# Kernel tuning notes

Hardware: AMD Instinct MI355X
Metric: run time of the kernel (lower is better)

## Reference

```python
import jax, jax.numpy as jnp
import numpy as np

EPS = 1e-36
N, F, C = 1024, 128, 2
P_DIM, BOND, SPACING, M_DIM = 4, 32, 8, 16
EMB_DIM = P_DIM ** C  # 16
NORM_INTERVAL = 1
STD = 0.55
N_BIG = (F + SPACING - 1) // SPACING   # 16 sites with output leg m=M_DIM
N_SMALL = F - N_BIG                    # 112 sites with m=1


def trig_embedding(x, p):
    # x: [N, F, C] in [0,1] -> [N, F, p**C]
    half = p // 2
    ks = 2.0 ** jnp.arange(1, half + 1, dtype=x.dtype)   # [2, 4, ...]
    ang = jnp.pi * x[..., None] / ks                     # [N,F,C,half]
    emb = jnp.stack([jnp.sin(ang), jnp.cos(ang)], -1)    # [N,F,C,half,2] -> sin1,cos1,sin2,cos2,...
    emb = emb.reshape(x.shape + (p,)) / float(np.sqrt(half))
    cur = emb[..., 0, :]
    for c in range(1, x.shape[-1]):                      # tensor product over channels
        cur = (cur[..., :, None] * emb[..., c, None, :]).reshape(x.shape[0], x.shape[1], -1)
    return cur


def build_mpo(w_big, w_small, sites, spacing):
    # Reassemble per-site MPO tensors (Dl, e, m, Dr); boundary bonds sliced to 1.
    mpo = []
    for n in range(sites):
        A = w_big[n // spacing] if n % spacing == 0 else w_small[n - n // spacing - 1]
        if n == 0:
            A = A[:1]
        if n == sites - 1:
            A = A[..., :1]
        mpo.append(A)
    return mpo


def _rescale(cur, log_norm):
    s = jnp.max(jnp.abs(cur))
    return cur / s, log_norm + jnp.log(s + EPS)


def log_partition_mpo(mpo):
    # log of squared F-norm of the MPO via zig-zag self-contraction with rescaling.
    sites = len(mpo)
    cur = mpo[0][0]                                   # (e, m, r); left bond (=1) squeezed
    log_norm = jnp.zeros((), cur.dtype)
    for i in range(sites - 1):
        if NORM_INTERVAL is not None and i % NORM_INTERVAL == 0:
            cur, log_norm = _rescale(cur, log_norm)
        if i == 0:
            cur = jnp.einsum('emf,emg->fg', cur, mpo[0][0])      # contract phys legs of site 0 copies
        else:
            cur = jnp.einsum('demf,demg->fg', cur, mpo[i])       # absorb copy-chain site i
        cur = jnp.einsum('fg,femh->gemh', cur, mpo[i + 1])       # absorb original-chain site i+1
    cur = jnp.einsum('demf,demg->fg', cur, mpo[-1])              # (1,1)
    return jnp.log(cur.reshape(()) + EPS) + log_norm


def sample_logit(emb_row, mpo):
    # emb_row: [F, e]. psi_n = sum_e A_n[l,e,m,r] emb[n,e]; logit = log ||psi||^2 (zig-zag + rescale).
    sites = len(mpo)
    psi_prev = jnp.einsum('emr,e->mr', mpo[0][0], emb_row[0])
    cur = psi_prev
    log_norm = jnp.zeros((), cur.dtype)
    for i in range(sites - 1):
        if NORM_INTERVAL is not None and i % NORM_INTERVAL == 0:
            cur, log_norm = _rescale(cur, log_norm)
        if i == 0:
            cur = jnp.einsum('mf,mg->fg', cur, psi_prev)
        else:
            cur = jnp.einsum('dmf,dmg->fg', cur, psi_prev)
        psi_prev = jnp.einsum('lemr,e->lmr', mpo[i + 1], emb_row[i + 1])
        cur = jnp.einsum('fg,fmh->gmh', cur, psi_prev)
    cur = jnp.einsum('dmf,dmg->fg', cur, psi_prev)               # (1,1)
    return jnp.log(cur.reshape(()) + EPS) + log_norm


def forward(x, w_big, w_small):
    emb = trig_embedding(x, P_DIM)                    # [N, F, EMB_DIM]
    mpo = build_mpo(w_big, w_small, F, SPACING)
    log_Z = log_partition_mpo(mpo)
    logits = jax.vmap(lambda e: sample_logit(e, mpo))(emb)   # [N]
    return logits, log_Z


def setup_inputs() -> dict:
    key = jax.random.key(0)
    k1, k2, k3 = jax.random.split(key, 3)
    x = jax.random.uniform(k1, (N, F, C), dtype=jnp.float32)
    w_big = STD * jax.random.normal(k2, (N_BIG, BOND, EMB_DIM, M_DIM, BOND), dtype=jnp.float32)
    w_small = STD * jax.random.normal(k3, (N_SMALL, BOND, EMB_DIM, 1, BOND), dtype=jnp.float32)
    return {"x": x, "w_big": w_big, "w_small": w_small}


def reference(x, w_big, w_small):
    return forward(x, w_big, w_small)
```

## Files before the change

kernel.cpp:

```cpp
#include <hip/hip_runtime.h>

typedef __attribute__((ext_vector_type(8)))  short  s16x8;
typedef __attribute__((ext_vector_type(8)))  __bf16 bf16x8;
typedef __attribute__((ext_vector_type(16))) float  f32x16;
typedef __attribute__((ext_vector_type(4)))  unsigned int u32x4;

#define EPSF 1e-36f

static __device__ __forceinline__ f32x16 MFMA(s16x8 a, s16x8 b, f32x16 c) {
  return __builtin_amdgcn_mfma_f32_32x32x16_bf16(
      __builtin_bit_cast(bf16x8, a), __builtin_bit_cast(bf16x8, b), c, 0, 0, 0);
}

static __device__ __forceinline__ short f2bf(float f) {
  unsigned u = __builtin_bit_cast(unsigned, f);
  u = (u + 0x7FFFu + ((u >> 16) & 1u)) >> 16;
  return (short)u;
}

static __device__ __forceinline__ unsigned pkf(float a, float b) {
  return (unsigned)(unsigned short)f2bf(a) | ((unsigned)(unsigned short)f2bf(b) << 16);
}

static __device__ __forceinline__ void redistR(const f32x16 d, float sc, int h,
                                               s16x8& f0, s16x8& f1) {
  unsigned pk[8];
#pragma unroll
  for (int q = 0; q < 8; ++q) pk[q] = pkf(d[2 * q] * sc, d[2 * q + 1] * sc);
  unsigned s0 = h ? pk[0] : pk[2];
  unsigned s1 = h ? pk[1] : pk[3];
  unsigned s2 = h ? pk[4] : pk[6];
  unsigned s3 = h ? pk[5] : pk[7];
  unsigned r0 = (unsigned)__shfl_xor((int)s0, 32);
  unsigned r1 = (unsigned)__shfl_xor((int)s1, 32);
  unsigned r2 = (unsigned)__shfl_xor((int)s2, 32);
  unsigned r3 = (unsigned)__shfl_xor((int)s3, 32);
  u32x4 a, b;
  a.x = h ? r0 : pk[0]; a.y = h ? r1 : pk[1]; a.z = h ? pk[2] : r0; a.w = h ? pk[3] : r1;
  b.x = h ? r2 : pk[4]; b.y = h ? r3 : pk[5]; b.z = h ? pk[6] : r2; b.w = h ? pk[7] : r3;
  f0 = __builtin_bit_cast(s16x8, a);
  f1 = __builtin_bit_cast(s16x8, b);
}

static __device__ __forceinline__ void decodeStep(int sig, int& site, int& m, int& off) {
  int g = sig / 23, o = sig - g * 23;
  if (o < 16) { site = 8 * g; m = o; off = g * 376832 + o * 16384; }
  else { site = 8 * g + (o - 15); m = 0; off = g * 376832 + 262144 + (o - 16) * 16384; }
}

extern "C" __global__ void prep_emb_k(const float* __restrict__ x, float* __restrict__ Em) {
  int id = blockIdx.x * 256 + threadIdx.x;
  int site = id >> 10, n = id & 1023;
  float x0 = x[(n * 128 + site) * 2 + 0];
  float x1 = x[(n * 128 + site) * 2 + 1];
  const float P5 = 1.57079632679f, P25 = 0.785398163397f, R = 0.70710678118f;
  float u[4] = {sinf(P5 * x0) * R, cosf(P5 * x0) * R, sinf(P25 * x0) * R, cosf(P25 * x0) * R};
  float v[4] = {sinf(P5 * x1) * R, cosf(P5 * x1) * R, sinf(P25 * x1) * R, cosf(P25 * x1) * R};
#pragma unroll
  for (int a = 0; a < 4; ++a) {
    float4 o;
    o.x = u[a] * v[0]; o.y = u[a] * v[1]; o.z = u[a] * v[2]; o.w = u[a] * v[3];
    *(float4*)&Em[id * 16 + a * 4] = o;
  }
}

extern "C" __global__ void prep_w_k(const float* __restrict__ wb, const float* __restrict__ wsm,
                                    short* __restrict__ As, short* __restrict__ As2) {
  int site = blockIdx.x;
  bool big = (site & 7) == 0;
  int nE = big ? 262144 : 16384;
  int nb = (site + 7) >> 3;
  int bs = nb * 262144 + (site - nb) * 16384;
  int kb = site >> 3;
  int ksm = site - kb - 1;
  for (int i = threadIdx.x; i < nE; i += 256) {
    int e = i & 15, r = (i >> 4) & 31, l = (i >> 9) & 31, m = i >> 14;
    float val = big ? wb[(((kb * 32 + l) * 16 + e) * 16 + m) * 32 + r]
                    : wsm[((ksm * 32 + l) * 16 + e) * 32 + r];
    if (site == 0 && l != 0) val = 0.f;
    if (site == 127 && r != 0) val = 0.f;
    short bv = f2bf(val);
    As2[bs + i] = bv;
    As[bs + ((m * 32 + r) * 16 + e) * 32 + l] = bv;
  }
}

extern "C" __global__ void __launch_bounds__(256, 1)
tn_main(const short* __restrict__ As, const short* __restrict__ As2,
        const float* __restrict__ Em, float* __restrict__ out) {
  __shared__ __align__(16) char smem[40960];
  const int tid = threadIdx.x;
  const int lane = tid & 63;
  const int w = tid >> 6;
  const int c31 = lane & 31;
  const int h = lane >> 5;
  const f32x16 Z = {0.f,0.f,0.f,0.f,0.f,0.f,0.f,0.f,0.f,0.f,0.f,0.f,0.f,0.f,0.f,0.f};

  if (blockIdx.x < 256) {
    const int n0 = blockIdx.x * 4;
    s16x8 Mf0 = {0,0,0,0,0,0,0,0}, Mf1 = {0,0,0,0,0,0,0,0};
    if (lane == 0) Mf0[0] = (short)0x3F80;
    f32x16 Macc = Z;
    float log_norm = 0.f;
    s16x8 Ef = {0,0,0,0,0,0,0,0};

    auto stage = [&](int sig2) {
      int st2, m2, off2; decodeStep(sig2, st2, m2, off2);
      const char* src = (const char*)As2 + (size_t)off2 * 2;
#pragma unroll
      for (int k = 0; k < 8; ++k) {
        int GL = (k * 4 + w) * 64 + lane;
        int gs = (GL & ~63) | ((GL & 63) ^ ((GL >> 6) & 7));
        __builtin_amdgcn_global_load_lds((const unsigned int*)(src + gs * 16),
                                         (unsigned int*)(smem + (k * 4 + w) * 1024),
                                         16, 0, 0);
      }
    };

    stage(0);
    __syncthreads();

#pragma unroll 1
    for (int sig = 0; sig < 368; ++sig) {
      int site, m, off; decodeStep(sig, site, m, off); (void)off;

      if (m == 0) {
        float4 q0 = {0.f,0.f,0.f,0.f}, q1 = {0.f,0.f,0.f,0.f};
        if (c31 < 4) {
          const float* ep = Em + ((size_t)site * 1024 + n0 + c31) * 16 + 8 * h;
          q0 = *(const float4*)ep;
          q1 = *(const float4*)(ep + 4);
        }
        u32x4 ef;
        ef.x = pkf(q0.x, q0.y); ef.y = pkf(q0.z, q0.w);
        ef.z = pkf(q1.x, q1.y); ef.w = pkf(q1.z, q1.w);
        Ef = __builtin_bit_cast(s16x8, ef);
      }

      unsigned* barea = (unsigned*)(smem + 32768);
#pragma unroll
      for (int t = 0; t < 4; ++t) {
        const int lA = 8 * w + 2 * t;
        const int lB = lA + 1;
        s16x8 WA = *(const s16x8*)(smem + lA * 1024 + (((c31 * 2 + h) ^ (lA & 7)) << 4));
        s16x8 WB = *(const s16x8*)(smem + lB * 1024 + (((c31 * 2 + h) ^ (lB & 7)) << 4));
        f32x16 DA = MFMA(Ef, WA, Z);
        f32x16 DB = MFMA(Ef, WB, Z);
        if (h == 0) {
          const int pr = (4 * w + t) ^ (c31 & 15);
#pragma unroll
          for (int q = 0; q < 4; ++q)
            barea[q * 512 + c31 * 16 + pr] = pkf(DA[q], DB[q]);
        }
      }
      __syncthreads();

      if (sig + 1 < 368) stage(sig + 1);

      const unsigned* ba = (const unsigned*)(smem + 32768) + w * 512 + c31 * 16;
      u32x4 b0v, b1v;
#pragma unroll
      for (int i = 0; i < 4; ++i) ((unsigned*)&b0v)[i] = ba[(4 * h + i) ^ (c31 & 15)];
#pragma unroll
      for (int i = 0; i < 4; ++i) ((unsigned*)&b1v)[i] = ba[(8 + 4 * h + i) ^ (c31 & 15)];
      s16x8 c0 = __builtin_bit_cast(s16x8, b0v);
      s16x8 c1 = __builtin_bit_cast(s16x8, b1v);

      f32x16 D1 = MFMA(Mf0, c0, Z);
      D1 = MFMA(Mf1, c1, D1);
      s16x8 Cf0, Cf1;
      redistR(D1, 1.f, h, Cf0, Cf1);
      if (m == 0) Macc = Z;
      Macc = MFMA(c0, Cf0, Macc);
      Macc = MFMA(c1, Cf1, Macc);

      bool lastM = (m == (((site & 7) == 0) ? 15 : 0));
      if (lastM) {
        if (site < 127) {
          float s = fabsf(Macc[0]);
#pragma unroll
          for (int j = 1; j < 16; ++j) s = fmaxf(s, fabsf(Macc[j]));
#pragma unroll
          for (int off2 = 32; off2 >= 1; off2 >>= 1) s = fmaxf(s, __shfl_xor(s, off2));
          float inv = 1.f / (s + EPSF);
          log_norm += logf(s + EPSF);
          redistR(Macc, inv, h, Mf0, Mf1);
        } else {
          if (lane == 0) out[n0 + w] = logf(fmaxf(Macc[0], 0.f) + EPSF) + log_norm;
        }
      }
      __syncthreads();
    }
  } else {
    float* red = (float*)smem;
    s16x8 Mf0 = {0,0,0,0,0,0,0,0}, Mf1 = {0,0,0,0,0,0,0,0};
    if (lane == 0) Mf0[0] = (short)0x3F80;
    f32x16 Macc = Z;
    float log_norm = 0.f;
#pragma unroll 1
    for (int sig = 0; sig < 368; ++sig) {
      int site, m, off; decodeStep(sig, site, m, off);
      if (m == 0) Macc = Z;
      s16x8 pa[4], pb[4];
#pragma unroll
      for (int q = 0; q < 4; ++q) {
        int e = 4 * w + q;
        const short* ap = As + off + (c31 * 16 + e) * 32;
        pa[q] = *(const s16x8*)(ap + 8 * h);
        pb[q] = *(const s16x8*)(ap + 16 + 8 * h);
      }
#pragma unroll
      for (int q = 0; q < 4; ++q) {
        f32x16 D1 = MFMA(Mf0, pa[q], Z);
        D1 = MFMA(Mf1, pb[q], D1);
        s16x8 Cf0, Cf1;
        redistR(D1, 1.f, h, Cf0, Cf1);
        Macc = MFMA(pa[q], Cf0, Macc);
        Macc = MFMA(pb[q], Cf1, Macc);
      }
      bool lastM = (m == (((site & 7) == 0) ? 15 : 0));
      if (lastM) {
        float* myr = red + w * 1056;
#pragma unroll
        for (int reg = 0; reg < 16; ++reg) {
          int row = (reg & 3) + 8 * (reg >> 2) + 4 * h;
          myr[row * 33 + c31] = Macc[reg];
        }
        __syncthreads();
        f32x16 tot;
#pragma unroll
        for (int reg = 0; reg < 16; ++reg) {
          int row = (reg & 3) + 8 * (reg >> 2) + 4 * h;
          int idx = row * 33 + c31;
          tot[reg] = red[idx] + red[1056 + idx] + red[2112 + idx] + red[3168 + idx];
        }
        float s = fabsf(tot[0]);
#pragma unroll
        for (int j = 1; j < 16; ++j) s = fmaxf(s, fabsf(tot[j]));
#pragma unroll
        for (int off2 = 32; off2 >= 1; off2 >>= 1) s = fmaxf(s, __shfl_xor(s, off2));
        __syncthreads();
        if (site < 127) {
          float inv = 1.f / (s + EPSF);
          log_norm += logf(s + EPSF);
          redistR(tot, inv, h, Mf0, Mf1);
        } else {
          if (tid == 0) out[1024] = logf(fmaxf(tot[0], 0.f) + EPSF) + log_norm;
        }
      }
    }
  }
}

extern "C" void kernel_launch(void* const* d_in, const int* in_sizes, int n_in,
                              void* d_out, int out_size, void* d_ws, size_t ws_size,
                              hipStream_t stream) {
  (void)in_sizes; (void)n_in; (void)out_size; (void)ws_size;
  const float* x   = (const float*)d_in[0];
  const float* wb  = (const float*)d_in[1];
  const float* wsm = (const float*)d_in[2];
  char* ws = (char*)d_ws;
  short* As  = (short*)ws;
  short* As2 = (short*)(ws + 12058624);
  float* Em  = (float*)(ws + 24117248);
  float* out = (float*)d_out;

  prep_emb_k<<<512, 256, 0, stream>>>(x, Em);
  prep_w_k<<<128, 256, 0, stream>>>(wb, wsm, As, As2);
  tn_main<<<257, 256, 0, stream>>>(As, As2, Em, out);
}
```

Measured before the change: 1.265 ms.

## Warp-specialize sample blocks into producer/consumer waves with double-buffered LDS

Blocks grow to 512 threads. In the sample blocks, four producer waves load MPO tiles into registers and compute the embedding-contracted slices into a double-buffered LDS area, while four consumer waves run the serial bond-chain MFMA updates one step behind. All embeddings for the block are preloaded into LDS up front, and the partition-function block now spreads its work over 8 waves with ping-pong partial buffers, so it needs one barrier per step instead of two. The aim is to hide global load latency and the producer MFMA work behind the serial consumer chain, at the cost of more registers, more LDS and a barrier every step.

Result: slower. 1.365 ms (+7.8%).

```diff
diff --git a/kernel.cpp b/kernel.cpp
--- a/kernel.cpp
+++ b/kernel.cpp
@@ -85,10 +85,10 @@
   }
 }
 
-extern "C" __global__ void __launch_bounds__(256, 1)
+extern "C" __global__ void __launch_bounds__(512, 1)
 tn_main(const short* __restrict__ As, const short* __restrict__ As2,
         const float* __restrict__ Em, float* __restrict__ out) {
-  __shared__ __align__(16) char smem[40960];
+  __shared__ __align__(16) char smem[67584];
   const int tid = threadIdx.x;
   const int lane = tid & 63;
   const int w = tid >> 6;
@@ -97,150 +97,175 @@
   const f32x16 Z = {0.f,0.f,0.f,0.f,0.f,0.f,0.f,0.f,0.f,0.f,0.f,0.f,0.f,0.f,0.f,0.f};
 
   if (blockIdx.x < 256) {
+    unsigned* bufU = (unsigned*)smem;
+    float* EmL = (float*)(smem + 16384);
     const int n0 = blockIdx.x * 4;
+
+    {
+      float4* dst = (float4*)EmL;
+#pragma unroll
+      for (int k = 0; k < 4; ++k) {
+        int j = k * 512 + tid;
+        int st = j >> 4, s = (j >> 2) & 3, q = j & 3;
+        dst[j] = *((const float4*)(Em + ((size_t)st * 1024 + n0 + s) * 16) + q);
+      }
+    }
+    __syncthreads();
+
+    if (w < 4) {
+      s16x8 Mf0 = {0,0,0,0,0,0,0,0}, Mf1 = {0,0,0,0,0,0,0,0};
+      if (lane == 0) Mf0[0] = (short)0x3F80;
+      f32x16 Macc = Z;
+      float log_norm = 0.f;
+
+      __syncthreads();
+#pragma unroll 1
+      for (int sig = 0; sig < 368; ++sig) {
+        int site, m, off; decodeStep(sig, site, m, off); (void)off;
+        const unsigned* bu = bufU + (sig & 1) * 2048 + w * 512 + c31;
+        u32x4 b0v, b1v;
+#pragma unroll
+        for (int j = 0; j < 4; ++j) ((unsigned*)&b0v)[j] = bu[(4 * h + j) * 32];
+#pragma unroll
+        for (int j = 0; j < 4; ++j) ((unsigned*)&b1v)[j] = bu[(8 + 4 * h + j) * 32];
+        s16x8 c0 = __builtin_bit_cast(s16x8, b0v);
+        s16x8 c1 = __builtin_bit_cast(s16x8, b1v);
+
+        f32x16 D1 = MFMA(Mf0, c0, Z);
+        D1 = MFMA(Mf1, c1, D1);
+        s16x8 Cf0, Cf1;
+        redistR(D1, 1.f, h, Cf0, Cf1);
+        if (m == 0) Macc = Z;
+        Macc = MFMA(c0, Cf0, Macc);
+        Macc = MFMA(c1, Cf1, Macc);
+
+        bool lastM = (m == (((site & 7) == 0) ? 15 : 0));
+        if (lastM) {
+          if (site < 127) {
+            float s = fabsf(Macc[0]);
+#pragma unroll
+            for (int j = 1; j < 16; ++j) s = fmaxf(s, fabsf(Macc[j]));
+#pragma unroll
+            for (int off2 = 32; off2 >= 1; off2 >>= 1) s = fmaxf(s, __shfl_xor(s, off2));
+            float inv = 1.f / (s + EPSF);
+            log_norm += logf(s + EPSF);
+            redistR(Macc, inv, h, Mf0, Mf1);
+          } else {
+            if (lane == 0) out[n0 + w] = logf(fmaxf(Macc[0], 0.f) + EPSF) + log_norm;
+          }
+        }
+        __syncthreads();
+      }
+    } else {
+      const int pw = w - 4;
+      s16x8 Ef = {0,0,0,0,0,0,0,0};
+      int curSite = -1;
+      s16x8 W0[8], W1[8];
+
+      auto loadW = [&](int sigN, s16x8* W) {
+        int st, mm, off; decodeStep(sigN, st, mm, off);
+        const short* base = As2 + off + ((8 * pw) * 32 + c31) * 16 + 8 * h;
+#pragma unroll
+        for (int t = 0; t < 8; ++t) W[t] = *(const s16x8*)(base + t * 512);
+      };
+
+      auto produce = [&](int sigN, const s16x8* W) {
+        int st, mm, off; decodeStep(sigN, st, mm, off); (void)off;
+        if (mm == 0 && st != curSite) {
+          curSite = st;
+          float4 q0 = {0.f,0.f,0.f,0.f}, q1 = {0.f,0.f,0.f,0.f};
+          if (c31 < 4) {
+            const float4* ep = (const float4*)(EmL + (st * 4 + c31) * 16);
+            q0 = ep[2 * h];
+            q1 = ep[2 * h + 1];
+          }
+          u32x4 ef;
+          ef.x = pkf(q0.x, q0.y); ef.y = pkf(q0.z, q0.w);
+          ef.z = pkf(q1.x, q1.y); ef.w = pkf(q1.z, q1.w);
+          Ef = __builtin_bit_cast(s16x8, ef);
+        }
+        unsigned* bw = bufU + (sigN & 1) * 2048;
+#pragma unroll
+        for (int u = 0; u < 4; ++u) {
+          f32x16 DA = MFMA(Ef, W[2 * u], Z);
+          f32x16 DB = MFMA(Ef, W[2 * u + 1], Z);
+          if (h == 0) {
+            const int l2 = 4 * pw + u;
+#pragma unroll
+            for (int q = 0; q < 4; ++q)
+              bw[q * 512 + l2 * 32 + c31] = pkf(DA[q], DB[q]);
+          }
+        }
+      };
+
+      loadW(0, W0);
+      loadW(1, W1);
+      produce(0, W0);
+      __syncthreads();
+
+#pragma unroll 1
+      for (int sig = 0; sig < 368; sig += 2) {
+        if (sig + 2 < 368) loadW(sig + 2, W0);
+        produce(sig + 1, W1);
+        __syncthreads();
+        if (sig + 3 < 368) loadW(sig + 3, W1);
+        if (sig + 2 < 368) produce(sig + 2, W0);
+        __syncthreads();
+      }
+    }
+  } else {
+    float* part = (float*)smem;
     s16x8 Mf0 = {0,0,0,0,0,0,0,0}, Mf1 = {0,0,0,0,0,0,0,0};
     if (lane == 0) Mf0[0] = (short)0x3F80;
-    f32x16 Macc = Z;
+    f32x16 Pacc = Z;
     float log_norm = 0.f;
-    s16x8 Ef = {0,0,0,0,0,0,0,0};
-
-    auto stage = [&](int sig2) {
-      int st2, m2, off2; decodeStep(sig2, st2, m2, off2);
-      const char* src = (const char*)As2 + (size_t)off2 * 2;
-#pragma unroll
-      for (int k = 0; k < 8; ++k) {
-        int GL = (k * 4 + w) * 64 + lane;
-        int gs = (GL & ~63) | ((GL & 63) ^ ((GL >> 6) & 7));
-        __builtin_amdgcn_global_load_lds((const unsigned int*)(src + gs * 16),
-                                         (unsigned int*)(smem + (k * 4 + w) * 1024),
-                                         16, 0, 0);
-      }
-    };
-
-    stage(0);
+
     __syncthreads();
-
-#pragma unroll 1
-    for (int sig = 0; sig < 368; ++sig) {
-      int site, m, off; decodeStep(sig, site, m, off); (void)off;
-
-      if (m == 0) {
-        float4 q0 = {0.f,0.f,0.f,0.f}, q1 = {0.f,0.f,0.f,0.f};
-        if (c31 < 4) {
-          const float* ep = Em + ((size_t)site * 1024 + n0 + c31) * 16 + 8 * h;
-          q0 = *(const float4*)ep;
-          q1 = *(const float4*)(ep + 4);
-        }
-        u32x4 ef;
-        ef.x = pkf(q0.x, q0.y); ef.y = pkf(q0.z, q0.w);
-        ef.z = pkf(q1.x, q1.y); ef.w = pkf(q1.z, q1.w);
-        Ef = __builtin_bit_cast(s16x8, ef);
-      }
-
-      unsigned* barea = (unsigned*)(smem + 32768);
-#pragma unroll
-      for (int t = 0; t < 4; ++t) {
-        const int lA = 8 * w + 2 * t;
-        const int lB = lA + 1;
-        s16x8 WA = *(const s16x8*)(smem + lA * 1024 + (((c31 * 2 + h) ^ (lA & 7)) << 4));
-        s16x8 WB = *(const s16x8*)(smem + lB * 1024 + (((c31 * 2 + h) ^ (lB & 7)) << 4));
-        f32x16 DA = MFMA(Ef, WA, Z);
-        f32x16 DB = MFMA(Ef, WB, Z);
-        if (h == 0) {
-          const int pr = (4 * w + t) ^ (c31 & 15);
-#pragma unroll
-          for (int q = 0; q < 4; ++q)
-            barea[q * 512 + c31 * 16 + pr] = pkf(DA[q], DB[q]);
-        }
-      }
-      __syncthreads();
-
-      if (sig + 1 < 368) stage(sig + 1);
-
-      const unsigned* ba = (const unsigned*)(smem + 32768) + w * 512 + c31 * 16;
-      u32x4 b0v, b1v;
-#pragma unroll
-      for (int i = 0; i < 4; ++i) ((unsigned*)&b0v)[i] = ba[(4 * h + i) ^ (c31 & 15)];
-#pragma unroll
-      for (int i = 0; i < 4; ++i) ((unsigned*)&b1v)[i] = ba[(8 + 4 * h + i) ^ (c31 & 15)];
-      s16x8 c0 = __builtin_bit_cast(s16x8, b0v);
-      s16x8 c1 = __builtin_bit_cast(s16x8, b1v);
-
-      f32x16 D1 = MFMA(Mf0, c0, Z);
-      D1 = MFMA(Mf1, c1, D1);
-      s16x8 Cf0, Cf1;
-      redistR(D1, 1.f, h, Cf0, Cf1);
-      if (m == 0) Macc = Z;
-      Macc = MFMA(c0, Cf0, Macc);
-      Macc = MFMA(c1, Cf1, Macc);
-
-      bool lastM = (m == (((site & 7) == 0) ? 15 : 0));
-      if (lastM) {
-        if (site < 127) {
-          float s = fabsf(Macc[0]);
-#pragma unroll
-          for (int j = 1; j < 16; ++j) s = fmaxf(s, fabsf(Macc[j]));
-#pragma unroll
-          for (int off2 = 32; off2 >= 1; off2 >>= 1) s = fmaxf(s, __shfl_xor(s, off2));
-          float inv = 1.f / (s + EPSF);
-          log_norm += logf(s + EPSF);
-          redistR(Macc, inv, h, Mf0, Mf1);
-        } else {
-          if (lane == 0) out[n0 + w] = logf(fmaxf(Macc[0], 0.f) + EPSF) + log_norm;
-        }
-      }
-      __syncthreads();
-    }
-  } else {
-    float* red = (float*)smem;
-    s16x8 Mf0 = {0,0,0,0,0,0,0,0}, Mf1 = {0,0,0,0,0,0,0,0};
-    if (lane == 0) Mf0[0] = (short)0x3F80;
-    f32x16 Macc = Z;
-    float log_norm = 0.f;
 #pragma unroll 1
     for (int sig = 0; sig < 368; ++sig) {
       int site, m, off; decodeStep(sig, site, m, off);
-      if (m == 0) Macc = Z;
-      s16x8 pa[4], pb[4];
-#pragma unroll
-      for (int q = 0; q < 4; ++q) {
-        int e = 4 * w + q;
+      if (m == 0) Pacc = Z;
+#pragma unroll
+      for (int q = 0; q < 2; ++q) {
+        int e = 2 * w + q;
         const short* ap = As + off + (c31 * 16 + e) * 32;
-        pa[q] = *(const s16x8*)(ap + 8 * h);
-        pb[q] = *(const s16x8*)(ap + 16 + 8 * h);
-      }
-#pragma unroll
-      for (int q = 0; q < 4; ++q) {
-        f32x16 D1 = MFMA(Mf0, pa[q], Z);
-        D1 = MFMA(Mf1, pb[q], D1);
+        s16x8 pa = *(const s16x8*)(ap + 8 * h);
+        s16x8 pb = *(const s16x8*)(ap + 16 + 8 * h);
+        f32x16 D1 = MFMA(Mf0, pa, Z);
+        D1 = MFMA(Mf1, pb, D1);
         s16x8 Cf0, Cf1;
         redistR(D1, 1.f, h, Cf0, Cf1);
-        Macc = MFMA(pa[q], Cf0, Macc);
-        Macc = MFMA(pb[q], Cf1, Macc);
+        Pacc = MFMA(pa, Cf0, Pacc);
+        Pacc = MFMA(pb, Cf1, Pacc);
       }
       bool lastM = (m == (((site & 7) == 0) ? 15 : 0));
       if (lastM) {
-        float* myr = red + w * 1056;
+        float* myr = part + ((site & 1) * 8 + w) * 1056;
 #pragma unroll
         for (int reg = 0; reg < 16; ++reg) {
           int row = (reg & 3) + 8 * (reg >> 2) + 4 * h;
-          myr[row * 33 + c31] = Macc[reg];
-        }
-        __syncthreads();
+          myr[row * 33 + c31] = Pacc[reg];
+        }
+      }
+      __syncthreads();
+      if (lastM) {
+        const float* base = part + (site & 1) * 8 * 1056;
         f32x16 tot;
 #pragma unroll
         for (int reg = 0; reg < 16; ++reg) {
           int row = (reg & 3) + 8 * (reg >> 2) + 4 * h;
           int idx = row * 33 + c31;
-          tot[reg] = red[idx] + red[1056 + idx] + red[2112 + idx] + red[3168 + idx];
-        }
-        float s = fabsf(tot[0]);
-#pragma unroll
-        for (int j = 1; j < 16; ++j) s = fmaxf(s, fabsf(tot[j]));
-#pragma unroll
-        for (int off2 = 32; off2 >= 1; off2 >>= 1) s = fmaxf(s, __shfl_xor(s, off2));
-        __syncthreads();
+          float sum = 0.f;
+#pragma unroll
+          for (int w2 = 0; w2 < 8; ++w2) sum += base[w2 * 1056 + idx];
+          tot[reg] = sum;
+        }
         if (site < 127) {
+          float s = fabsf(tot[0]);
+#pragma unroll
+          for (int j = 1; j < 16; ++j) s = fmaxf(s, fabsf(tot[j]));
+#pragma unroll
+          for (int off2 = 32; off2 >= 1; off2 >>= 1) s = fmaxf(s, __shfl_xor(s, off2));
           float inv = 1.f / (s + EPSF);
           log_norm += logf(s + EPSF);
           redistR(tot, inv, h, Mf0, Mf1);
@@ -267,5 +292,5 @@
 
   prep_emb_k<<<512, 256, 0, stream>>>(x, Em);
   prep_w_k<<<128, 256, 0, stream>>>(wb, wsm, As, As2);
-  tn_main<<<257, 256, 0, stream>>>(As, As2, Em, out);
-}
+  tn_main<<<257, 512, 0, stream>>>(As, As2, Em, out);
+}
```
